# Kernel tuning notes

Measured on AMD Instinct MI355X. Metric: run time of the kernel, lower is better.

The kernel has to match this reference:

```python
import jax, jax.numpy as jnp
import numpy as np

EMBED_DIM = 1024
ATTN_DIM = 1024
BATCH = 4
SEQ = 2048


def setup_inputs() -> dict:
    key = jax.random.key(0)
    k1, k2, k3, k4 = jax.random.split(key, 4)
    embedded = jax.random.normal(k1, (BATCH, SEQ, EMBED_DIM), dtype=jnp.float32)
    # torch Linear weights have shape [out_features, in_features]
    scale = 1.0 / np.sqrt(EMBED_DIM)
    W_K = jax.random.uniform(k2, (ATTN_DIM, EMBED_DIM), dtype=jnp.float32, minval=-scale, maxval=scale)
    W_Q = jax.random.uniform(k3, (ATTN_DIM, EMBED_DIM), dtype=jnp.float32, minval=-scale, maxval=scale)
    W_V = jax.random.uniform(k4, (ATTN_DIM, EMBED_DIM), dtype=jnp.float32, minval=-scale, maxval=scale)
    return {"embedded": embedded, "W_K": W_K, "W_Q": W_Q, "W_V": W_V}


def reference(embedded, W_K, W_Q, W_V):
    # embedded: [B, L, E]; W_*: [A, E] (torch Linear layout, applied as x @ W.T)
    L = embedded.shape[1]
    A = W_K.shape[0]
    K = jnp.einsum('ble,ae->bla', embedded, W_K)
    Q = jnp.einsum('ble,ae->bla', embedded, W_Q)
    V = jnp.einsum('ble,ae->bla', embedded, W_V)
    att = jnp.einsum('bqa,bka->bqk', Q, K) / jnp.sqrt(jnp.float32(A))  # [B, L, L]
    causal = jnp.tril(jnp.ones((L, L), dtype=bool))  # lower-triangular mask
    att = jnp.where(causal, att, -jnp.inf)
    att = jax.nn.softmax(att, axis=-1)
    return jnp.einsum('bqk,bka->bqa', att, V)
```

## Files before the change

### kernel.cpp

```cpp
#include <hip/hip_runtime.h>
#include <hip/hip_bf16.h>
#include <stdint.h>

#define BATCH 4
#define SEQ   2048
#define EMB   1024
#define ADIM  1024

typedef __attribute__((ext_vector_type(8))) short  short8;
typedef __attribute__((ext_vector_type(4))) float  float4v;

static __device__ __forceinline__ unsigned short f2bf(float f) {
    unsigned int u = __float_as_uint(f);
    u += 0x7FFFu + ((u >> 16) & 1u);
    return (unsigned short)(u >> 16);
}

static __device__ __forceinline__ uint2 pack4(float4v v) {
    uint2 r;
    r.x = (unsigned)f2bf(v.x) | ((unsigned)f2bf(v.y) << 16);
    r.y = (unsigned)f2bf(v.z) | ((unsigned)f2bf(v.w) << 16);
    return r;
}

static __device__ __forceinline__ void gload16(const void* g, void* l) {
    __builtin_amdgcn_global_load_lds(
        (const __attribute__((address_space(1))) void*)g,
        (__attribute__((address_space(3))) void*)l, 16, 0, 0);
}

static __device__ __forceinline__ int swz8(int row) { return ((row >> 1) & 3) << 3; }

__global__ __launch_bounds__(256) void prep_kernel(
    const float* __restrict__ X,  const float* __restrict__ Wv,
    const float* __restrict__ Wq, const float* __restrict__ Wk,
    unsigned short* __restrict__ Xb, unsigned short* __restrict__ Wvb,
    unsigned short* __restrict__ WqT, unsigned short* __restrict__ WkT,
    float* __restrict__ rowsum, float* __restrict__ out)
{
    __shared__ unsigned short T[64][72];
    const int bI = blockIdx.x;
    if (bI < 4608) {
        const float* src; unsigned short* dst; int off;
        if (bI < 4096) { src = X;  dst = Xb;  off = bI; }
        else           { src = Wv; dst = Wvb; off = bI - 4096; }
        const int i = (off * 256 + threadIdx.x) * 8;
        float4v a = *(const float4v*)(src + i);
        float4v b = *(const float4v*)(src + i + 4);
        uint2 pa = pack4(a), pb = pack4(b);
        uint4 o; o.x = pa.x; o.y = pa.y; o.z = pb.x; o.w = pb.y;
        *(uint4*)(dst + i) = o;
        return;
    }
    if (bI < 4616) {
        const int i = ((bI - 4608) * 256 + threadIdx.x) * 4;
        *(float4v*)(rowsum + i) = float4v{0.f, 0.f, 0.f, 0.f};
        return;
    }
    if (bI >= 5128) {
        const int o   = bI - 5128;
        const int b   = o >> 10;
        const int blk = o & 1023;
        float* dst = out + ((size_t)(b * 2048 + 1024) * 1024)
                         + (size_t)blk * 1024 + threadIdx.x * 4;
        *(float4v*)dst = float4v{0.f, 0.f, 0.f, 0.f};
        return;
    }
    const int z    = (bI - 4616) >> 8;
    const int tile = (bI - 4616) & 255;
    const int ti = tile >> 4;
    const int tj = tile & 15;
    const float* W = z ? Wk : Wq;
    unsigned short* WT = z ? WkT : WqT;
    const int t  = threadIdx.x;
    const int r  = t >> 2;
    const int c  = (t & 3) << 4;

    const float* src = W + (size_t)(ti * 64 + r) * EMB + tj * 64 + c;
    #pragma unroll
    for (int u = 0; u < 4; ++u) {
        float4v v = *(const float4v*)(src + 4 * u);
        uint2 p = pack4(v);
        *(uint2*)&T[r][c + 4 * u] = p;
    }
    __syncthreads();
    unsigned short tmp[16];
    #pragma unroll
    for (int u = 0; u < 16; ++u) tmp[u] = T[c + u][r];
    unsigned short* dst = WT + (size_t)(tj * 64 + r) * EMB + ti * 64 + c;
    *(uint4*)(dst)     = *(uint4*)&tmp[0];
    *(uint4*)(dst + 8) = *(uint4*)&tmp[8];
}

static __device__ __forceinline__ void gemm_core(
    const unsigned short* __restrict__ A, const unsigned short* __restrict__ B,
    int lda, int ldb, int m0, int n0, int klen,
    unsigned short* As, unsigned short* Bs, float4v acc[4][4])
{
    const int tid  = threadIdx.x;
    const int r    = tid >> 2;
    const int c8   = ((tid & 3) << 3) ^ swz8(tid >> 2);
    const int lane = tid & 63;
    const int wave = tid >> 6;
    const int quad = lane >> 4;
    const int l16  = lane & 15;
    const int wm   = (wave >> 1) << 6;
    const int wn   = (wave & 1) << 6;

    const unsigned short* Ag = A + (size_t)(m0 + r) * lda + c8;
    const unsigned short* Bg = B + (size_t)(n0 + r) * ldb + c8;
    unsigned short* Al = As + tid * 8;
    unsigned short* Bl = Bs + tid * 8;
    const int niter = klen >> 5;

    #define ISSUE(k0, st) do { \
        unsigned short* al_ = Al + (st) * 4096; \
        unsigned short* bl_ = Bl + (st) * 4096; \
        gload16(Ag + (k0),                    al_); \
        gload16(Ag + (k0) + (size_t)64 * lda, al_ + 2048); \
        gload16(Bg + (k0),                    bl_); \
        gload16(Bg + (k0) + (size_t)64 * ldb, bl_ + 2048); \
    } while (0)

    ISSUE(0, 0);
    ISSUE(32, 1);

    int ci = 0, ii = 2;
    for (int it = 0; it < niter; ++it) {
        const int knext = (it + 2 < niter) ? ((it + 2) << 5) : 0;
        ISSUE(knext, ii);
        asm volatile("s_waitcnt vmcnt(8)" ::: "memory");
        asm volatile("s_barrier" ::: "memory");

        const unsigned short* Ah = As + ci * 4096;
        const unsigned short* Bh = Bs + ci * 4096;
        short8 af[4], bfr[4];
        #pragma unroll
        for (int i = 0; i < 4; ++i) {
            const int row = wm + 16 * i + l16;
            af[i] = *(const short8*)&Ah[row * 32 + ((quad * 8) ^ swz8(row))];
        }
        #pragma unroll
        for (int j = 0; j < 4; ++j) {
            const int row = wn + 16 * j + l16;
            bfr[j] = *(const short8*)&Bh[row * 32 + ((quad * 8) ^ swz8(row))];
        }
        #pragma unroll
        for (int i = 0; i < 4; ++i)
            #pragma unroll
            for (int j = 0; j < 4; ++j)
                acc[i][j] = __builtin_amdgcn_mfma_f32_16x16x32_bf16(af[i], bfr[j], acc[i][j], 0, 0, 0);

        asm volatile("s_barrier" ::: "memory");
        ci = (ci == 2) ? 0 : ci + 1;
        ii = (ii == 2) ? 0 : ii + 1;
    }
    asm volatile("s_waitcnt vmcnt(0)" ::: "memory");
    #undef ISSUE
}

#define DECL_TILE_IDX() \
    const int lane = threadIdx.x & 63; \
    const int wave = threadIdx.x >> 6; \
    const int quad = lane >> 4; \
    const int l16  = lane & 15; \
    const int wm   = (wave >> 1) << 6; \
    const int wn   = (wave & 1) << 6;

__global__ __launch_bounds__(256, 3) void m_kernel(
    const unsigned short* __restrict__ WkT, const unsigned short* __restrict__ WqT,
    float* __restrict__ Mtf)
{
    __shared__ __align__(16) unsigned short As[3 * 128 * 32];
    __shared__ __align__(16) unsigned short Bs[3 * 128 * 32];
    const int idx = blockIdx.x;
    const int kc  = idx >> 6;
    const int t   = idx & 63;
    const int m0  = (t >> 3) << 7;
    const int n0  = (t & 7) << 7;

    float4v acc[4][4];
    #pragma unroll
    for (int i = 0; i < 4; ++i)
        #pragma unroll
        for (int j = 0; j < 4; ++j)
            acc[i][j] = float4v{0.f, 0.f, 0.f, 0.f};

    gemm_core(WkT + kc * 256, WqT + kc * 256, EMB, EMB, m0, n0, 256, As, Bs, acc);

    float* dst = Mtf + (size_t)kc * 1024 * 1024;
    DECL_TILE_IDX();
    #pragma unroll
    for (int i = 0; i < 4; ++i)
        #pragma unroll
        for (int j = 0; j < 4; ++j)
            #pragma unroll
            for (int rr = 0; rr < 4; ++rr) {
                const int row = m0 + wm + 16 * i + quad * 4 + rr;
                const int col = n0 + wn + 16 * j + l16;
                dst[(size_t)row * EMB + col] = acc[i][j][rr];
            }
}

__global__ __launch_bounds__(256) void mc_kernel(
    const float* __restrict__ Mtf, unsigned short* __restrict__ Mt)
{
    const int base = (blockIdx.x * 256 + threadIdx.x) * 16;
    #pragma unroll
    for (int u = 0; u < 4; ++u) {
        const int i = base + u * 4;
        float4v s = *(const float4v*)(Mtf + i);
        s = s + *(const float4v*)(Mtf + 1048576 + i);
        s = s + *(const float4v*)(Mtf + 2097152 + i);
        s = s + *(const float4v*)(Mtf + 3145728 + i);
        s = s * 0.03125f;
        uint2 p = pack4(s);
        *(uint2*)(Mt + i) = p;
    }
}

__global__ __launch_bounds__(512, 2) void qv_kernel(
    const unsigned short* __restrict__ Xb, const unsigned short* __restrict__ Mt,
    const unsigned short* __restrict__ Wvb,
    unsigned short* __restrict__ Qpb, unsigned short* __restrict__ Vtb)
{
    __shared__ __align__(16) unsigned short LDS[49152];
    unsigned short* As = LDS;
    unsigned short* Bs = LDS + 24576;

    const int idx  = blockIdx.x;
    const int mt   = ((idx & 7) << 2) | ((idx >> 3) & 3);
    const int slot = idx >> 5;
    const int z    = slot >> 2;
    const int n0   = (slot & 3) << 8;
    const int m0   = mt << 8;
    const unsigned short* B = z ? Wvb : Mt;

    const int tid  = threadIdx.x;
    const int lane = tid & 63;
    const int wave = tid >> 6;
    const int quad = lane >> 4;
    const int l16  = lane & 15;
    const int wm   = (wave >> 2) << 7;
    const int wn   = (wave & 3) << 6;

    const int srow = tid >> 2;
    const int c8   = ((tid & 3) << 3) ^ swz8(srow);

    const unsigned short* Ag0 = Xb + (size_t)(m0 + srow) * EMB + c8;
    const unsigned short* Ag1 = Ag0 + (size_t)128 * EMB;
    const unsigned short* Bg0 = B  + (size_t)(n0 + srow) * EMB + c8;
    const unsigned short* Bg1 = Bg0 + (size_t)128 * EMB;
    unsigned short* Al = As + tid * 8;
    unsigned short* Bl = Bs + tid * 8;

    #define ISSUE_QA(t, st) do { \
        gload16(Ag0 + (t) * 32, Al + (st) * 8192); \
        gload16(Ag1 + (t) * 32, Al + (st) * 8192 + 4096); \
    } while (0)
    #define ISSUE_QB(t, st) do { \
        gload16(Bg0 + (t) * 32, Bl + (st) * 8192); \
        gload16(Bg1 + (t) * 32, Bl + (st) * 8192 + 4096); \
    } while (0)

    float4v acc[8][4];
    #pragma unroll
    for (int i = 0; i < 8; ++i)
        #pragma unroll
        for (int j = 0; j < 4; ++j)
            acc[i][j] = float4v{0.f, 0.f, 0.f, 0.f};

    ISSUE_QA(0, 0); ISSUE_QB(0, 0);
    ISSUE_QA(1, 1); ISSUE_QB(1, 1);

    int ci = 0, ii = 2;
    for (int it = 0; it < 32; ++it) {
        const unsigned short* Ah = As + ci * 8192;
        const unsigned short* Bh = Bs + ci * 8192;
        short8 bfr[4];

        if (it + 2 < 32) ISSUE_QA(it + 2, ii);
        asm volatile("s_waitcnt vmcnt(6)" ::: "memory");
        asm volatile("s_barrier" ::: "memory");
        {
            short8 af[4];
            #pragma unroll
            for (int i = 0; i < 4; ++i) {
                const int row = wm + 16 * i + l16;
                af[i] = *(const short8*)&Ah[row * 32 + ((quad * 8) ^ swz8(row))];
            }
            #pragma unroll
            for (int j = 0; j < 4; ++j) {
                const int row = wn + 16 * j + l16;
                bfr[j] = *(const short8*)&Bh[row * 32 + ((quad * 8) ^ swz8(row))];
            }
            __builtin_amdgcn_s_setprio(1);
            #pragma unroll
            for (int i = 0; i < 4; ++i)
                #pragma unroll
                for (int j = 0; j < 4; ++j)
                    acc[i][j] = __builtin_amdgcn_mfma_f32_16x16x32_bf16(af[i], bfr[j], acc[i][j], 0, 0, 0);
            __builtin_amdgcn_s_setprio(0);
        }
        asm volatile("s_barrier" ::: "memory");

        if (it + 2 < 32) ISSUE_QB(it + 2, ii);
        {
            short8 af[4];
            #pragma unroll
            for (int i = 0; i < 4; ++i) {
                const int row = wm + 64 + 16 * i + l16;
                af[i] = *(const short8*)&Ah[row * 32 + ((quad * 8) ^ swz8(row))];
            }
            __builtin_amdgcn_s_setprio(1);
            #pragma unroll
            for (int i = 0; i < 4; ++i)
                #pragma unroll
                for (int j = 0; j < 4; ++j)
                    acc[i + 4][j] = __builtin_amdgcn_mfma_f32_16x16x32_bf16(af[i], bfr[j], acc[i + 4][j], 0, 0, 0);
            __builtin_amdgcn_s_setprio(0);
        }
        asm volatile("s_barrier" ::: "memory");
        ci = (ci == 2) ? 0 : ci + 1;
        ii = (ii == 2) ? 0 : ii + 1;
    }
    asm volatile("s_waitcnt vmcnt(0)" ::: "memory");
    #undef ISSUE_QA
    #undef ISSUE_QB

    if (z == 0) {
        #pragma unroll
        for (int i = 0; i < 8; ++i)
            #pragma unroll
            for (int j = 0; j < 4; ++j)
                #pragma unroll
                for (int rr = 0; rr < 4; ++rr) {
                    const int row = m0 + wm + ((i & 3) << 4) + ((i >> 2) << 6) + quad * 4 + rr;
                    const int col = n0 + wn + 16 * j + l16;
                    Qpb[(size_t)row * ADIM + col] = f2bf(acc[i][j][rr]);
                }
    } else {
        const int bb = m0 >> 11;
        const int l0 = m0 & (SEQ - 1);
        #pragma unroll
        for (int h = 0; h < 2; ++h) {
            __syncthreads();
            if ((wm >> 7) == h) {
                #pragma unroll
                for (int i = 0; i < 8; ++i)
                    #pragma unroll
                    for (int j = 0; j < 4; ++j) {
                        const int qloc = ((i & 3) << 4) + ((i >> 2) << 6) + quad * 4;
                        const int acol = wn + 16 * j + l16;
                        uint2 w;
                        w.x = (unsigned)f2bf(acc[i][j][0]) | ((unsigned)f2bf(acc[i][j][1]) << 16);
                        w.y = (unsigned)f2bf(acc[i][j][2]) | ((unsigned)f2bf(acc[i][j][3]) << 16);
                        *(uint2*)&LDS[acol * 136 + qloc] = w;
                    }
            }
            __syncthreads();
            const int acol = tid >> 1;
            const int qh   = (tid & 1) << 6;
            unsigned short* dst = Vtb + (((size_t)(bb * ADIM + n0 + acol)) << 11)
                                      + l0 + h * 128 + qh;
            #pragma unroll
            for (int u = 0; u < 8; ++u)
                *(uint4*)(dst + u * 8) = *(const uint4*)&LDS[acol * 136 + qh + u * 8];
        }
    }
}

__global__ __launch_bounds__(256, 3) void s_kernel(
    const unsigned short* __restrict__ Qpb, const unsigned short* __restrict__ Xb,
    unsigned short* __restrict__ E, float* __restrict__ rowsum)
{
    const int idx = blockIdx.x;
    const int x   = idx & 7;
    const int j   = idx >> 3;
    const int b   = j / 17;
    const int u   = j - b * 17;
    const int qt  = (u <= x) ? x : 15 - x;
    const int kt  = (u <= x) ? u : u - (x + 1);
    const int q0  = qt << 7;
    const int k0  = kt << 7;

    __shared__ __align__(16) unsigned short As[3 * 128 * 32];
    __shared__ __align__(16) unsigned short Bs[3 * 128 * 32];

    float4v acc[4][4];
    #pragma unroll
    for (int i = 0; i < 4; ++i)
        #pragma unroll
        for (int jj = 0; jj < 4; ++jj)
            acc[i][jj] = float4v{0.f, 0.f, 0.f, 0.f};

    gemm_core(Qpb + (size_t)b * SEQ * ADIM, Xb + (size_t)b * SEQ * EMB,
              ADIM, EMB, q0, k0, EMB, As, Bs, acc);

    unsigned short* Eb = E + (size_t)b * SEQ * SEQ;
    float* rsb = rowsum + (size_t)b * SEQ;
    DECL_TILE_IDX();
    #pragma unroll
    for (int i = 0; i < 4; ++i)
        #pragma unroll
        for (int rr = 0; rr < 4; ++rr) {
            const int row = q0 + wm + 16 * i + quad * 4 + rr;
            float s = 0.f;
            #pragma unroll
            for (int jj = 0; jj < 4; ++jj) {
                const int col = k0 + wn + 16 * jj + l16;
                float e = (col <= row) ? __expf(acc[i][jj][rr]) : 0.f;
                s += e;
                Eb[(size_t)row * SEQ + col] = f2bf(e);
            }
            s += __shfl_xor(s, 1);
            s += __shfl_xor(s, 2);
            s += __shfl_xor(s, 4);
            s += __shfl_xor(s, 8);
            if (l16 == 0) atomicAdd(&rsb[row], s);
        }
}

__global__ __launch_bounds__(256, 3) void pv_kernel(
    const unsigned short* __restrict__ E, const unsigned short* __restrict__ Vtb,
    const float* __restrict__ rowsum, float* __restrict__ out)
{
    const int idx  = blockIdx.x;
    const int x    = idx & 7;
    const int j    = idx >> 3;
    const int slot = j >> 5;
    const int c    = j & 31;
    const int b    = c >> 3;
    const int a0   = (c & 7) << 7;

    int qt, kbeg, klen, dual;
    if (slot == 0)      { qt = x;      kbeg = 0;    klen = (x + 1) << 7; dual = 0; }
    else if (slot == 1) { qt = 15 - x; kbeg = 0;    klen = 1024;         dual = 1; }
    else                { qt = 15 - x; kbeg = 1024; klen = (8 - x) << 7; dual = 1; }
    const int q0 = qt << 7;

    __shared__ __align__(16) unsigned short As[3 * 128 * 32];
    __shared__ __align__(16) unsigned short Bs[3 * 128 * 32];

    float4v acc[4][4];
    #pragma unroll
    for (int i = 0; i < 4; ++i)
        #pragma unroll
        for (int jj = 0; jj < 4; ++jj)
            acc[i][jj] = float4v{0.f, 0.f, 0.f, 0.f};

    gemm_core(E + (size_t)b * SEQ * SEQ + kbeg, Vtb + (size_t)b * ADIM * SEQ + kbeg,
              SEQ, SEQ, q0, a0, klen, As, Bs, acc);

    float* ob = out + (size_t)b * SEQ * ADIM;
    const float* rsb = rowsum + (size_t)b * SEQ;
    DECL_TILE_IDX();
    if (!dual) {
        #pragma unroll
        for (int i = 0; i < 4; ++i)
            #pragma unroll
            for (int rr = 0; rr < 4; ++rr) {
                const int row = q0 + wm + 16 * i + quad * 4 + rr;
                const float inv = 1.0f / rsb[row];
                #pragma unroll
                for (int jj = 0; jj < 4; ++jj) {
                    const int col = a0 + wn + 16 * jj + l16;
                    ob[(size_t)row * ADIM + col] = acc[i][jj][rr] * inv;
                }
            }
    } else {
        #pragma unroll
        for (int i = 0; i < 4; ++i)
            #pragma unroll
            for (int rr = 0; rr < 4; ++rr) {
                const int row = q0 + wm + 16 * i + quad * 4 + rr;
                const float inv = 1.0f / rsb[row];
                #pragma unroll
                for (int jj = 0; jj < 4; ++jj) {
                    const int col = a0 + wn + 16 * jj + l16;
                    atomicAdd(&ob[(size_t)row * ADIM + col], acc[i][jj][rr] * inv);
                }
            }
    }
}

extern "C" void kernel_launch(void* const* d_in, const int* in_sizes, int n_in,
                              void* d_out, int out_size, void* d_ws, size_t ws_size,
                              hipStream_t stream)
{
    const float* X  = (const float*)d_in[0];
    const float* Wk = (const float*)d_in[1];
    const float* Wq = (const float*)d_in[2];
    const float* Wv = (const float*)d_in[3];
    float* out = (float*)d_out;

    const size_t MB = 1024 * 1024;
    char* ws = (char*)d_ws;
    unsigned short* Xb  = (unsigned short*)(ws);
    unsigned short* Wvb = (unsigned short*)(ws + 16 * MB);
    unsigned short* WqT = (unsigned short*)(ws + 18 * MB);
    unsigned short* WkT = (unsigned short*)(ws + 20 * MB);
    unsigned short* Mt  = (unsigned short*)(ws + 22 * MB);
    unsigned short* Qpb = (unsigned short*)(ws + 24 * MB);
    unsigned short* E   = (unsigned short*)(ws + 40 * MB);
    unsigned short* Vtb = (unsigned short*)(ws + 72 * MB);
    float*          rowsum = (float*)(ws + 88 * MB);
    float*          Mtf = (float*)(ws + 40 * MB);

    hipLaunchKernelGGL(prep_kernel, dim3(9224), dim3(256), 0, stream,
                       X, Wv, Wq, Wk, Xb, Wvb, WqT, WkT, rowsum, out);
    hipLaunchKernelGGL(m_kernel, dim3(256), dim3(256), 0, stream, WkT, WqT, Mtf);
    hipLaunchKernelGGL(mc_kernel, dim3(256), dim3(256), 0, stream, Mtf, Mt);
    hipLaunchKernelGGL(qv_kernel, dim3(256), dim3(512), 0, stream,
                       Xb, Mt, Wvb, Qpb, Vtb);
    hipLaunchKernelGGL(s_kernel, dim3(544), dim3(256), 0, stream, Qpb, Xb, E, rowsum);
    hipLaunchKernelGGL(pv_kernel, dim3(768), dim3(256), 0, stream, E, Vtb, rowsum, out);
}
```

Measured before the change: 231.5 us.

## Drop split-K atomics in PV and simplify causal tile scheduling

The PV kernel stops splitting long query tiles into two K halves that are combined with atomicAdd. Each block now computes a full causal K range and writes output directly, launching 512 blocks with the heaviest tiles first. The prep kernel no longer zeroes half of the output. The S kernel switches from paired load-balanced tile mapping to a plain triangular index with batch interleaving. The main QV GEMM loop now always issues the prefetch, using a dummy tile near the end, to remove a branch. This removes atomic traffic and output zeroing, but the PV blocks become very unbalanced (1 to 16 K-tiles each), which risks a long tail.

```diff
diff --git a/kernel.cpp b/kernel.cpp
--- a/kernel.cpp
+++ b/kernel.cpp
@@ -36,7 +36,7 @@
     const float* __restrict__ Wq, const float* __restrict__ Wk,
     unsigned short* __restrict__ Xb, unsigned short* __restrict__ Wvb,
     unsigned short* __restrict__ WqT, unsigned short* __restrict__ WkT,
-    float* __restrict__ rowsum, float* __restrict__ out)
+    float* __restrict__ rowsum)
 {
     __shared__ unsigned short T[64][72];
     const int bI = blockIdx.x;
@@ -57,15 +57,6 @@
         *(float4v*)(rowsum + i) = float4v{0.f, 0.f, 0.f, 0.f};
         return;
     }
-    if (bI >= 5128) {
-        const int o   = bI - 5128;
-        const int b   = o >> 10;
-        const int blk = o & 1023;
-        float* dst = out + ((size_t)(b * 2048 + 1024) * 1024)
-                         + (size_t)blk * 1024 + threadIdx.x * 4;
-        *(float4v*)dst = float4v{0.f, 0.f, 0.f, 0.f};
-        return;
-    }
     const int z    = (bI - 4616) >> 8;
     const int tile = (bI - 4616) & 255;
     const int ti = tile >> 4;
@@ -275,11 +266,12 @@
 
     int ci = 0, ii = 2;
     for (int it = 0; it < 32; ++it) {
+        const int tn = (it + 2 < 32) ? (it + 2) : 0;
         const unsigned short* Ah = As + ci * 8192;
         const unsigned short* Bh = Bs + ci * 8192;
         short8 bfr[4];
 
-        if (it + 2 < 32) ISSUE_QA(it + 2, ii);
+        ISSUE_QA(tn, ii);
         asm volatile("s_waitcnt vmcnt(6)" ::: "memory");
         asm volatile("s_barrier" ::: "memory");
         {
@@ -304,7 +296,7 @@
         }
         asm volatile("s_barrier" ::: "memory");
 
-        if (it + 2 < 32) ISSUE_QB(it + 2, ii);
+        ISSUE_QB(tn, ii);
         {
             short8 af[4];
             #pragma unroll
@@ -375,14 +367,13 @@
     unsigned short* __restrict__ E, float* __restrict__ rowsum)
 {
     const int idx = blockIdx.x;
-    const int x   = idx & 7;
-    const int j   = idx >> 3;
-    const int b   = j / 17;
-    const int u   = j - b * 17;
-    const int qt  = (u <= x) ? x : 15 - x;
-    const int kt  = (u <= x) ? u : u - (x + 1);
-    const int q0  = qt << 7;
-    const int k0  = kt << 7;
+    const int b   = idx & 3;
+    const int tri = idx >> 2;
+    int qt = 0;
+    while (((qt + 1) * (qt + 2)) / 2 <= tri) ++qt;
+    const int kt = tri - (qt * (qt + 1)) / 2;
+    const int q0 = qt << 7;
+    const int k0 = kt << 7;
 
     __shared__ __align__(16) unsigned short As[3 * 128 * 32];
     __shared__ __align__(16) unsigned short Bs[3 * 128 * 32];
@@ -391,8 +382,8 @@
     #pragma unroll
     for (int i = 0; i < 4; ++i)
         #pragma unroll
-        for (int jj = 0; jj < 4; ++jj)
-            acc[i][jj] = float4v{0.f, 0.f, 0.f, 0.f};
+        for (int j = 0; j < 4; ++j)
+            acc[i][j] = float4v{0.f, 0.f, 0.f, 0.f};
 
     gemm_core(Qpb + (size_t)b * SEQ * ADIM, Xb + (size_t)b * SEQ * EMB,
               ADIM, EMB, q0, k0, EMB, As, Bs, acc);
@@ -407,9 +398,9 @@
             const int row = q0 + wm + 16 * i + quad * 4 + rr;
             float s = 0.f;
             #pragma unroll
-            for (int jj = 0; jj < 4; ++jj) {
-                const int col = k0 + wn + 16 * jj + l16;
-                float e = (col <= row) ? __expf(acc[i][jj][rr]) : 0.f;
+            for (int j = 0; j < 4; ++j) {
+                const int col = k0 + wn + 16 * j + l16;
+                float e = (col <= row) ? __expf(acc[i][j][rr]) : 0.f;
                 s += e;
                 Eb[(size_t)row * SEQ + col] = f2bf(e);
             }
@@ -425,19 +416,12 @@
     const unsigned short* __restrict__ E, const unsigned short* __restrict__ Vtb,
     const float* __restrict__ rowsum, float* __restrict__ out)
 {
-    const int idx  = blockIdx.x;
-    const int x    = idx & 7;
-    const int j    = idx >> 3;
-    const int slot = j >> 5;
-    const int c    = j & 31;
-    const int b    = c >> 3;
-    const int a0   = (c & 7) << 7;
-
-    int qt, kbeg, klen, dual;
-    if (slot == 0)      { qt = x;      kbeg = 0;    klen = (x + 1) << 7; dual = 0; }
-    else if (slot == 1) { qt = 15 - x; kbeg = 0;    klen = 1024;         dual = 1; }
-    else                { qt = 15 - x; kbeg = 1024; klen = (8 - x) << 7; dual = 1; }
-    const int q0 = qt << 7;
+    const int idx = blockIdx.x;
+    const int t   = (idx < 256) ? (15 - (idx >> 5)) : ((idx - 256) >> 5);
+    const int rem = idx & 31;
+    const int b   = rem >> 3;
+    const int a0  = (rem & 7) << 7;
+    const int q0  = t << 7;
 
     __shared__ __align__(16) unsigned short As[3 * 128 * 32];
     __shared__ __align__(16) unsigned short Bs[3 * 128 * 32];
@@ -446,42 +430,27 @@
     #pragma unroll
     for (int i = 0; i < 4; ++i)
         #pragma unroll
-        for (int jj = 0; jj < 4; ++jj)
-            acc[i][jj] = float4v{0.f, 0.f, 0.f, 0.f};
-
-    gemm_core(E + (size_t)b * SEQ * SEQ + kbeg, Vtb + (size_t)b * ADIM * SEQ + kbeg,
-              SEQ, SEQ, q0, a0, klen, As, Bs, acc);
+        for (int j = 0; j < 4; ++j)
+            acc[i][j] = float4v{0.f, 0.f, 0.f, 0.f};
+
+    gemm_core(E + (size_t)b * SEQ * SEQ, Vtb + (size_t)b * ADIM * SEQ,
+              SEQ, SEQ, q0, a0, q0 + 128, As, Bs, acc);
 
     float* ob = out + (size_t)b * SEQ * ADIM;
     const float* rsb = rowsum + (size_t)b * SEQ;
     DECL_TILE_IDX();
-    if (!dual) {
-        #pragma unroll
-        for (int i = 0; i < 4; ++i)
-            #pragma unroll
-            for (int rr = 0; rr < 4; ++rr) {
-                const int row = q0 + wm + 16 * i + quad * 4 + rr;
-                const float inv = 1.0f / rsb[row];
-                #pragma unroll
-                for (int jj = 0; jj < 4; ++jj) {
-                    const int col = a0 + wn + 16 * jj + l16;
-                    ob[(size_t)row * ADIM + col] = acc[i][jj][rr] * inv;
-                }
-            }
-    } else {
-        #pragma unroll
-        for (int i = 0; i < 4; ++i)
-            #pragma unroll
-            for (int rr = 0; rr < 4; ++rr) {
-                const int row = q0 + wm + 16 * i + quad * 4 + rr;
-                const float inv = 1.0f / rsb[row];
-                #pragma unroll
-                for (int jj = 0; jj < 4; ++jj) {
-                    const int col = a0 + wn + 16 * jj + l16;
-                    atomicAdd(&ob[(size_t)row * ADIM + col], acc[i][jj][rr] * inv);
-                }
-            }
-    }
+    #pragma unroll
+    for (int i = 0; i < 4; ++i)
+        #pragma unroll
+        for (int rr = 0; rr < 4; ++rr) {
+            const int row = q0 + wm + 16 * i + quad * 4 + rr;
+            const float inv = 1.0f / rsb[row];
+            #pragma unroll
+            for (int j = 0; j < 4; ++j) {
+                const int col = a0 + wn + 16 * j + l16;
+                ob[(size_t)row * ADIM + col] = acc[i][j][rr] * inv;
+            }
+        }
 }
 
 extern "C" void kernel_launch(void* const* d_in, const int* in_sizes, int n_in,
@@ -507,12 +476,12 @@
     float*          rowsum = (float*)(ws + 88 * MB);
     float*          Mtf = (float*)(ws + 40 * MB);
 
-    hipLaunchKernelGGL(prep_kernel, dim3(9224), dim3(256), 0, stream,
-                       X, Wv, Wq, Wk, Xb, Wvb, WqT, WkT, rowsum, out);
+    hipLaunchKernelGGL(prep_kernel, dim3(5128), dim3(256), 0, stream,
+                       X, Wv, Wq, Wk, Xb, Wvb, WqT, WkT, rowsum);
     hipLaunchKernelGGL(m_kernel, dim3(256), dim3(256), 0, stream, WkT, WqT, Mtf);
     hipLaunchKernelGGL(mc_kernel, dim3(256), dim3(256), 0, stream, Mtf, Mt);
     hipLaunchKernelGGL(qv_kernel, dim3(256), dim3(512), 0, stream,
                        Xb, Mt, Wvb, Qpb, Vtb);
-    hipLaunchKernelGGL(s_kernel, dim3(544), dim3(256), 0, stream, Qpb, Xb, E, rowsum);
-    hipLaunchKernelGGL(pv_kernel, dim3(768), dim3(256), 0, stream, E, Vtb, rowsum, out);
-}
+    hipLaunchKernelGGL(s_kernel, dim3(4 * 136), dim3(256), 0, stream, Qpb, Xb, E, rowsum);
+    hipLaunchKernelGGL(pv_kernel, dim3(512), dim3(256), 0, stream, E, Vtb, rowsum, out);
+}
```

Result: faster. 223.7 us (-3.4%).
